# Kernel tuning notes

Hardware: AMD Instinct MI355X
Metric: run time of the kernel (lower is better)

Reference implementation:

```python
import jax, jax.numpy as jnp
import numpy as np

N_NODES = 16384
HIDDEN = 128
N_SPECIES = 119


def setup_inputs() -> dict:
    key = jax.random.key(0)
    k1, k2, k3, k4 = jax.random.split(key, 4)
    h_prev = jax.random.normal(k1, (N_NODES, HIDDEN), dtype=jnp.float32)
    m_curr = jax.random.normal(k2, (N_NODES, HIDDEN), dtype=jnp.float32)
    # sorted species indices (fast indexed_linear path in the original module)
    atom_types = jnp.sort(jax.random.randint(k3, (N_NODES,), 0, N_SPECIES))
    # per-species weight, init randn / sqrt(hidden_dim) as in the torch module
    weight = jax.random.normal(k4, (N_SPECIES, HIDDEN * HIDDEN), dtype=jnp.float32) / jnp.sqrt(
        jnp.float32(HIDDEN)
    )
    return {"h_prev": h_prev, "m_curr": m_curr, "atom_types": atom_types, "weight": weight}


def reference(h_prev, m_curr, atom_types, weight):
    # h_new[i] = h_prev[i] + W[Z[i]] @ m_curr[i]
    D = h_prev.shape[-1]
    W = weight.reshape(weight.shape[0], D, D)        # (S, D, D)
    Wg = W[atom_types]                               # (N, D, D) indexed gather
    m_transformed = jnp.einsum("nij,nj->ni", Wg, m_curr)
    return h_prev + m_transformed
```

## Files before the change

### kernel.cpp

```cpp
#include <hip/hip_runtime.h>
#include <stdint.h>

#define HID 128

typedef __attribute__((ext_vector_type(8))) __bf16 bf16x8;
typedef __attribute__((ext_vector_type(4))) float floatx4;

__device__ inline bf16x8 load_cvt8(const float* __restrict__ p) {
    floatx4 v0 = *(const floatx4*)(p);
    floatx4 v1 = *(const floatx4*)(p + 4);
    bf16x8 r;
    r[0] = (__bf16)v0[0]; r[1] = (__bf16)v0[1];
    r[2] = (__bf16)v0[2]; r[3] = (__bf16)v0[3];
    r[4] = (__bf16)v1[0]; r[5] = (__bf16)v1[1];
    r[6] = (__bf16)v1[2]; r[7] = (__bf16)v1[3];
    return r;
}

__global__ __launch_bounds__(256, 4) void elem_update_kernel(
    const float* __restrict__ h_prev,
    const float* __restrict__ m_curr,
    const int* __restrict__ atom_types,
    const float* __restrict__ weight,
    float* __restrict__ out)
{
    const int tid  = threadIdx.x;
    const int lane = tid & 63;
    const int wave = tid >> 6;
    const int l15  = lane & 15;
    const int quad = lane >> 4;

    const int wg       = blockIdx.x * 4 + wave;
    const int row_tile = wg >> 2;
    const int cq       = wg & 3;
    const int r0       = row_tile * 16;
    const int c0       = cq * 32;

    const int t = atom_types[r0 + l15];

    int s = 0;
    while (s < 16) {
        const int z = __shfl(t, s);
        unsigned long long neq = __ballot(t != z);
        unsigned bits = (unsigned)(neq & 0xFFFFull) & ~((1u << (s + 1)) - 1u);
        const int e = bits ? (int)__builtin_ctz(bits) : 16;

        const float* __restrict__ Wz = weight + (size_t)z * HID * HID;

        floatx4 acc[2];
        #pragma unroll
        for (int nt = 0; nt < 2; ++nt) {
            #pragma unroll
            for (int r = 0; r < 4; ++r) {
                acc[nt][r] = h_prev[(size_t)(r0 + quad * 4 + r) * HID + c0 + nt * 16 + l15];
            }
        }

        #pragma unroll
        for (int kk = 0; kk < 4; ++kk) {
            bf16x8 a = load_cvt8(m_curr + (size_t)(r0 + l15) * HID + kk * 32 + quad * 8);
            #pragma unroll
            for (int nt = 0; nt < 2; ++nt) {
                bf16x8 b = load_cvt8(Wz + (size_t)(c0 + nt * 16 + l15) * HID + kk * 32 + quad * 8);
                acc[nt] = __builtin_amdgcn_mfma_f32_16x16x32_bf16(a, b, acc[nt], 0, 0, 0);
            }
        }

        #pragma unroll
        for (int nt = 0; nt < 2; ++nt) {
            #pragma unroll
            for (int r = 0; r < 4; ++r) {
                int row = quad * 4 + r;
                if (row >= s && row < e) {
                    size_t idx = (size_t)(r0 + row) * HID + c0 + nt * 16 + l15;
                    out[idx] = acc[nt][r];
                }
            }
        }
        s = e;
    }
}

extern "C" void kernel_launch(void* const* d_in, const int* in_sizes, int n_in,
                              void* d_out, int out_size, void* d_ws, size_t ws_size,
                              hipStream_t stream) {
    const float* h_prev     = (const float*)d_in[0];
    const float* m_curr     = (const float*)d_in[1];
    const int*   atom_types = (const int*)d_in[2];
    const float* weight     = (const float*)d_in[3];
    float*       out        = (float*)d_out;

    const int n_nodes = in_sizes[2];
    const int blocks  = n_nodes / 16;
    elem_update_kernel<<<blocks, 256, 0, stream>>>(h_prev, m_curr, atom_types, weight, out);
}
```

Baseline: 88.67 us.

## Stage per-species weight in LDS and share it across a 64-row block

Each block now handles 64 rows, with every wave covering all 128 output columns. The block cooperatively loads the species weight matrix, converted to bf16, into a swizzled LDS buffer once per species segment, instead of each wave gathering W slices from global memory per 16-row tile. The m_curr fragments are hoisted into registers before the segment loop. The aim is fewer redundant weight reads from global memory. In exchange it adds __syncthreads barriers, a 32KB LDS footprint, lower occupancy (launch bounds 2), and a serialised load of the whole W per segment even when a wave has no rows in it.

```diff
diff --git a/kernel.cpp b/kernel.cpp
--- a/kernel.cpp
+++ b/kernel.cpp
@@ -17,63 +17,80 @@
     return r;
 }
 
-__global__ __launch_bounds__(256, 4) void elem_update_kernel(
+__global__ __launch_bounds__(256, 2) void elem_update_kernel(
     const float* __restrict__ h_prev,
     const float* __restrict__ m_curr,
     const int* __restrict__ atom_types,
     const float* __restrict__ weight,
     float* __restrict__ out)
 {
+    __shared__ __attribute__((aligned(16))) unsigned short Wlds[HID * HID];
+
     const int tid  = threadIdx.x;
     const int lane = tid & 63;
     const int wave = tid >> 6;
     const int l15  = lane & 15;
     const int quad = lane >> 4;
 
-    const int wg       = blockIdx.x * 4 + wave;
-    const int row_tile = wg >> 2;
-    const int cq       = wg & 3;
-    const int r0       = row_tile * 16;
-    const int c0       = cq * 32;
+    const int blk_r0 = blockIdx.x * 64;
+    const int wr0    = blk_r0 + wave * 16;
 
-    const int t = atom_types[r0 + l15];
+    const int t = atom_types[blk_r0 + lane];
+
+    bf16x8 a[4];
+    #pragma unroll
+    for (int kk = 0; kk < 4; ++kk)
+        a[kk] = load_cvt8(m_curr + (size_t)(wr0 + l15) * HID + kk * 32 + quad * 8);
 
     int s = 0;
-    while (s < 16) {
+    while (s < 64) {
         const int z = __shfl(t, s);
         unsigned long long neq = __ballot(t != z);
-        unsigned bits = (unsigned)(neq & 0xFFFFull) & ~((1u << (s + 1)) - 1u);
-        const int e = bits ? (int)__builtin_ctz(bits) : 16;
+        unsigned long long bits = (s < 63) ? (neq & ~((2ull << s) - 1ull)) : 0ull;
+        const int e = bits ? (int)__builtin_ctzll(bits) : 64;
 
-        const float* __restrict__ Wz = weight + (size_t)z * HID * HID;
+        __syncthreads();
+        const float* __restrict__ Wz = weight + (size_t)z * (HID * HID);
+        #pragma unroll
+        for (int i = 0; i < 8; ++i) {
+            const int linear = i * 2048 + tid * 8;
+            const int row = linear >> 7;
+            const int col = linear & 127;
+            bf16x8 b = load_cvt8(Wz + linear);
+            const int chunk = (col >> 3) ^ (row & 15);
+            *(bf16x8*)((char*)Wlds + row * 256 + chunk * 16) = b;
+        }
+        __syncthreads();
 
-        floatx4 acc[2];
-        #pragma unroll
-        for (int nt = 0; nt < 2; ++nt) {
+        const int lo = (s > wave * 16) ? s : wave * 16;
+        const int hi = (e < wave * 16 + 16) ? e : wave * 16 + 16;
+        if (lo < hi) {
+            floatx4 acc[8];
             #pragma unroll
-            for (int r = 0; r < 4; ++r) {
-                acc[nt][r] = h_prev[(size_t)(r0 + quad * 4 + r) * HID + c0 + nt * 16 + l15];
+            for (int nt = 0; nt < 8; ++nt) {
+                #pragma unroll
+                for (int r = 0; r < 4; ++r) {
+                    acc[nt][r] = h_prev[(size_t)(wr0 + quad * 4 + r) * HID + nt * 16 + l15];
+                }
             }
-        }
-
-        #pragma unroll
-        for (int kk = 0; kk < 4; ++kk) {
-            bf16x8 a = load_cvt8(m_curr + (size_t)(r0 + l15) * HID + kk * 32 + quad * 8);
             #pragma unroll
-            for (int nt = 0; nt < 2; ++nt) {
-                bf16x8 b = load_cvt8(Wz + (size_t)(c0 + nt * 16 + l15) * HID + kk * 32 + quad * 8);
-                acc[nt] = __builtin_amdgcn_mfma_f32_16x16x32_bf16(a, b, acc[nt], 0, 0, 0);
+            for (int kk = 0; kk < 4; ++kk) {
+                #pragma unroll
+                for (int nt = 0; nt < 8; ++nt) {
+                    const int chunk = (kk * 4 + quad) ^ l15;
+                    bf16x8 b = *(const bf16x8*)((const char*)Wlds +
+                                                (nt * 16 + l15) * 256 + chunk * 16);
+                    acc[nt] = __builtin_amdgcn_mfma_f32_16x16x32_bf16(a[kk], b, acc[nt], 0, 0, 0);
+                }
             }
-        }
-
-        #pragma unroll
-        for (int nt = 0; nt < 2; ++nt) {
             #pragma unroll
-            for (int r = 0; r < 4; ++r) {
-                int row = quad * 4 + r;
-                if (row >= s && row < e) {
-                    size_t idx = (size_t)(r0 + row) * HID + c0 + nt * 16 + l15;
-                    out[idx] = acc[nt][r];
+            for (int nt = 0; nt < 8; ++nt) {
+                #pragma unroll
+                for (int r = 0; r < 4; ++r) {
+                    const int brow = wave * 16 + quad * 4 + r;
+                    if (brow >= lo && brow < hi) {
+                        out[(size_t)(blk_r0 + brow) * HID + nt * 16 + l15] = acc[nt][r];
+                    }
                 }
             }
         }
@@ -91,6 +108,6 @@
     float*       out        = (float*)d_out;
 
     const int n_nodes = in_sizes[2];
-    const int blocks  = n_nodes / 16;
+    const int blocks  = n_nodes / 64;
     elem_update_kernel<<<blocks, 256, 0, stream>>>(h_prev, m_curr, atom_types, weight, out);
 }
```

Result: faster. 79.10 us (-10.8%).
